# Optimization experiments

Hardware: AMD Instinct MI355X
Metric: run time of the kernel (lower is better)

Reference implementation:

```python
import jax, jax.numpy as jnp
import numpy as np

IN_F, OUT_F, NG = 2048, 8192, 16
EPS = 1e-5

def setup_inputs() -> dict:
    key = jax.random.key(0)
    k = jax.random.split(key, 6)
    x = jax.random.normal(k[0], (4096, IN_F), dtype=jnp.float32)
    W = jax.random.normal(k[1], (OUT_F, IN_F), dtype=jnp.float32) * (1.0 / np.sqrt(IN_F))
    b = jax.random.normal(k[2], (OUT_F,), dtype=jnp.float32) * 0.01
    gn_w = jnp.ones((OUT_F,), dtype=jnp.float32)
    gn_b = jnp.zeros((OUT_F,), dtype=jnp.float32)
    mult_w = jax.random.normal(k[3], (OUT_F,), dtype=jnp.float32)
    return {"x": x, "W": W, "b": b, "gn_w": gn_w, "gn_b": gn_b, "mult_w": mult_w}

def reference(x, W, b, gn_w, gn_b, mult_w):
    B = x.shape[0]
    y = x @ W.T + b  # [B, OUT_F]
    g = y.reshape(B, NG, OUT_F // NG)
    mean = jnp.mean(g, axis=-1, keepdims=True)
    var = jnp.mean(jnp.square(g - mean), axis=-1, keepdims=True)
    n = ((g - mean) * jax.lax.rsqrt(var + EPS)).reshape(B, OUT_F)
    n = n * gn_w + gn_b
    s1 = n * jax.nn.sigmoid(n)
    m = s1 * mult_w
    return m * jax.nn.sigmoid(m)
```

## Files before the change

kernel.cpp:

```cpp
#include <hip/hip_runtime.h>

#define M_DIM 4096
#define N_DIM 8192
#define K_DIM 2048
#define NGRP 16
#define GSZ 512
#define EPSV 1e-5f

#define NX (M_DIM * K_DIM)
#define NW (N_DIM * K_DIM)
#define NY ((size_t)M_DIM * N_DIM)

typedef __attribute__((ext_vector_type(8))) short bf16x8;
typedef __attribute__((ext_vector_type(4))) float f32x4;
typedef __attribute__((ext_vector_type(8))) short shortx8;

__device__ __forceinline__ float b2f(short u) {
    union { unsigned u32; float f; } c;
    c.u32 = ((unsigned)(unsigned short)u) << 16;
    return c.f;
}

__device__ __forceinline__ short f2b(float f) {
    union { float f; unsigned u; } c; c.f = f;
    unsigned r = (c.u + 0x7fffu + ((c.u >> 16) & 1u)) >> 16;
    return (short)r;
}

__global__ __launch_bounds__(256) void convert_kernel(
    const float* __restrict__ x, const float* __restrict__ W,
    short* __restrict__ dst)
{
    const size_t base = ((size_t)blockIdx.x * 256 + threadIdx.x) * 32;
    const float* src = (base < NX) ? (x + base) : (W + (base - NX));
    f32x4 v[8];
#pragma unroll
    for (int c = 0; c < 8; ++c) v[c] = *(const f32x4*)(src + c * 4);
#pragma unroll
    for (int c = 0; c < 4; ++c) {
        shortx8 o;
#pragma unroll
        for (int j = 0; j < 4; ++j) {
            o[j]     = f2b(v[2 * c][j]);
            o[j + 4] = f2b(v[2 * c + 1][j]);
        }
        *(shortx8*)(dst + base + c * 8) = o;
    }
}

#define BKS 32
#define NTILES (K_DIM / BKS)

__global__ __launch_bounds__(512, 2) void gemm256_bf16_kernel(
    const short* __restrict__ A, const short* __restrict__ W, short* __restrict__ C)
{
    __shared__ __align__(16) short lds[4 * 16384];

    const int tid  = threadIdx.x;
    const int lane = tid & 63;
    const int wave = tid >> 6;
    const int wr   = wave >> 2;
    const int wc   = wave & 3;

    const unsigned orig = blockIdx.x;
    const unsigned swz  = (orig & 7) * 64 + (orig >> 3);
    const int blockCol = (swz & 31) * 256;
    const int blockRow = (swz >> 5) * 256;

    const int q0 = tid, q1 = tid + 512;
    const int sr0 = q0 >> 2, sc0 = (q0 & 3) ^ ((q0 >> 3) & 3);
    const int sr1 = q1 >> 2, sc1 = (q1 & 3) ^ ((q1 >> 3) & 3);
    const int offA0 = (blockRow + sr0) * K_DIM + sc0 * 8;
    const int offA1 = (blockRow + sr1) * K_DIM + sc1 * 8;
    const int offB0 = (blockCol + sr0) * K_DIM + sc0 * 8;
    const int offB1 = (blockCol + sr1) * K_DIM + sc1 * 8;

    const int fr    = lane & 15;
    const int pbyte = ((lane >> 4) ^ ((fr >> 1) & 3)) * 16;
    const int aBase = (wr * 128 + fr) * 64 + pbyte;
    const int bBase = (wc * 64  + fr) * 64 + pbyte;

    f32x4 acc[8][4] = {};
    bf16x8 af[8], bf[4];

    auto gll = [&](const short* g, short* l) {
        __builtin_amdgcn_global_load_lds(
            (const __attribute__((address_space(1))) void*)g,
            (__attribute__((address_space(3))) void*)l, 16, 0, 0);
    };
    auto stage1 = [&](int t, int k) {
        short* dA = lds + (t & 3) * 16384;
        short* dB = dA + 8192;
        const int ko = t * BKS;
        if (k == 0)      gll(A + offA0 + ko, dA + q0 * 8);
        else if (k == 1) gll(W + offB0 + ko, dB + q0 * 8);
        else if (k == 2) gll(A + offA1 + ko, dA + q1 * 8);
        else             gll(W + offB1 + ko, dB + q1 * 8);
    };
    auto bar = [&]() {
        __builtin_amdgcn_sched_barrier(0);
        __builtin_amdgcn_s_barrier();
        __builtin_amdgcn_sched_barrier(0);
    };
    auto mf = [&](int ib, int jb) {
        __builtin_amdgcn_s_setprio(1);
#pragma unroll
        for (int i = 0; i < 4; ++i)
#pragma unroll
            for (int j = 0; j < 2; ++j)
                acc[ib + i][jb + j] = __builtin_amdgcn_mfma_f32_16x16x32_bf16(
                    af[ib + i], bf[jb + j], acc[ib + i][jb + j], 0, 0, 0);
        __builtin_amdgcn_s_setprio(0);
    };

    auto subtile = [&](int t, int tstage, bool dostage, int vm) {
        const char* bA = (const char*)lds + (t & 3) * 32768;
        const char* bB = bA + 16384;
        af[0] = *(const bf16x8*)(bA + aBase);
        af[1] = *(const bf16x8*)(bA + aBase + 1024);
        af[2] = *(const bf16x8*)(bA + aBase + 2048);
        af[3] = *(const bf16x8*)(bA + aBase + 3072);
        bf[0] = *(const bf16x8*)(bB + bBase);
        bf[1] = *(const bf16x8*)(bB + bBase + 1024);
        if (dostage) stage1(tstage, 0);
        bar(); mf(0, 0); bar();
        bf[2] = *(const bf16x8*)(bB + bBase + 2048);
        bf[3] = *(const bf16x8*)(bB + bBase + 3072);
        if (dostage) stage1(tstage, 1);
        bar(); mf(0, 2); bar();
        af[4] = *(const bf16x8*)(bA + aBase + 4096);
        af[5] = *(const bf16x8*)(bA + aBase + 5120);
        af[6] = *(const bf16x8*)(bA + aBase + 6144);
        af[7] = *(const bf16x8*)(bA + aBase + 7168);
        if (dostage) stage1(tstage, 2);
        bar(); mf(4, 0); bar();
        if (dostage) stage1(tstage, 3);
        if (vm == 4)      asm volatile("s_waitcnt vmcnt(4)" ::: "memory");
        else if (vm == 0) asm volatile("s_waitcnt vmcnt(0)" ::: "memory");
        bar(); mf(4, 2); bar();
    };

    stage1(0, 0); stage1(0, 1); stage1(0, 2); stage1(0, 3);
    stage1(1, 0); stage1(1, 1); stage1(1, 2); stage1(1, 3);
    asm volatile("s_waitcnt vmcnt(4)" ::: "memory");
    bar();

    for (int i = 0; i < 31; ++i) {
        const int t0 = 2 * i;
        subtile(t0,     t0 + 2, true, 4);
        subtile(t0 + 1, t0 + 3, true, 4);
    }
    subtile(62, 0, false, 0);
    subtile(63, 0, false, -1);

    const int er = (lane >> 4) * 4;
    const int ec = lane & 15;
#pragma unroll
    for (int i = 0; i < 8; ++i) {
        const int rr = blockRow + wr * 128 + i * 16 + er;
#pragma unroll
        for (int j = 0; j < 4; ++j) {
            const int cc = blockCol + wc * 64 + j * 16 + ec;
#pragma unroll
            for (int r = 0; r < 4; ++r)
                C[(size_t)(rr + r) * N_DIM + cc] = f2b(acc[i][j][r]);
        }
    }
}

__global__ __launch_bounds__(256) void gn_silu_bf16_kernel(
    const short* __restrict__ Y,
    const float* __restrict__ bias,
    const float* __restrict__ gnw,
    const float* __restrict__ gnb,
    const float* __restrict__ mw,
    float* __restrict__ out)
{
    const int lane = threadIdx.x & 63;
    const int wave = threadIdx.x >> 6;
    const unsigned gid = blockIdx.x * 4u + wave;
    const unsigned row = gid >> 4;
    const unsigned grp = gid & 15;
    const int col = grp * GSZ + lane * 8;
    const size_t off = (size_t)row * N_DIM + col;

    bf16x8 v = *(const bf16x8*)(Y + off);
    f32x4 b0 = *(const f32x4*)(bias + col);
    f32x4 b1 = *(const f32x4*)(bias + col + 4);

    float y[8];
    float s = 0.f, s2 = 0.f;
#pragma unroll
    for (int j = 0; j < 8; ++j) {
        y[j] = b2f(v[j]) + (j < 4 ? b0[j] : b1[j - 4]);
        s  += y[j];
        s2 += y[j] * y[j];
    }
#pragma unroll
    for (int d = 1; d < 64; d <<= 1) {
        s  += __shfl_xor(s,  d, 64);
        s2 += __shfl_xor(s2, d, 64);
    }
    const float mean = s * (1.0f / GSZ);
    const float var  = s2 * (1.0f / GSZ) - mean * mean;
    const float inv  = rsqrtf(var + EPSV);

    f32x4 w0 = *(const f32x4*)(gnw + col);
    f32x4 w1 = *(const f32x4*)(gnw + col + 4);
    f32x4 g0 = *(const f32x4*)(gnb + col);
    f32x4 g1 = *(const f32x4*)(gnb + col + 4);
    f32x4 m0 = *(const f32x4*)(mw + col);
    f32x4 m1 = *(const f32x4*)(mw + col + 4);

    f32x4 o0, o1;
#pragma unroll
    for (int j = 0; j < 8; ++j) {
        float gwv = j < 4 ? w0[j] : w1[j - 4];
        float gbv = j < 4 ? g0[j] : g1[j - 4];
        float mwv = j < 4 ? m0[j] : m1[j - 4];
        float n  = (y[j] - mean) * inv * gwv + gbv;
        float s1 = n / (1.f + __expf(-n));
        float m  = s1 * mwv;
        float r  = m / (1.f + __expf(-m));
        if (j < 4) o0[j] = r; else o1[j - 4] = r;
    }
    *(f32x4*)(out + off)     = o0;
    *(f32x4*)(out + off + 4) = o1;
}

__global__ __launch_bounds__(256) void gemm_bt_f32_kernel(
    const float* __restrict__ A, const float* __restrict__ W, float* __restrict__ C)
{
    __shared__ __align__(16) short ldsA[128 * 32];
    __shared__ __align__(16) short ldsB[128 * 32];

    const int tid  = threadIdx.x;
    const int lane = tid & 63;
    const int wave = tid >> 6;
    const int blockRow = blockIdx.y * 128;
    const int blockCol = blockIdx.x * 128;
    const int srow = tid >> 1;
    const int scol = (tid & 1) * 16;
    const int wm  = (wave >> 1) * 64;
    const int wn  = (wave & 1) * 64;
    const int fr  = lane & 15;
    const int fko = (lane >> 4) * 8;

    f32x4 acc[4][4] = {};
    const size_t aRowOff = (size_t)(blockRow + srow) * K_DIM;
    const size_t wRowOff = (size_t)(blockCol + srow) * K_DIM;

    for (int k0 = 0; k0 < K_DIM; k0 += 32) {
        f32x4 va0 = *(const f32x4*)(A + aRowOff + k0 + scol);
        f32x4 va1 = *(const f32x4*)(A + aRowOff + k0 + scol + 4);
        f32x4 va2 = *(const f32x4*)(A + aRowOff + k0 + scol + 8);
        f32x4 va3 = *(const f32x4*)(A + aRowOff + k0 + scol + 12);
        f32x4 vb0 = *(const f32x4*)(W + wRowOff + k0 + scol);
        f32x4 vb1 = *(const f32x4*)(W + wRowOff + k0 + scol + 4);
        f32x4 vb2 = *(const f32x4*)(W + wRowOff + k0 + scol + 8);
        f32x4 vb3 = *(const f32x4*)(W + wRowOff + k0 + scol + 12);
        bf16x8 a0, a1, b0, b1;
#pragma unroll
        for (int j = 0; j < 4; ++j) {
            a0[j] = f2b(va0[j]); a0[j + 4] = f2b(va1[j]);
            a1[j] = f2b(va2[j]); a1[j + 4] = f2b(va3[j]);
            b0[j] = f2b(vb0[j]); b0[j + 4] = f2b(vb1[j]);
            b1[j] = f2b(vb2[j]); b1[j + 4] = f2b(vb3[j]);
        }
        *(bf16x8*)(ldsA + srow * 32 + scol)     = a0;
        *(bf16x8*)(ldsA + srow * 32 + scol + 8) = a1;
        *(bf16x8*)(ldsB + srow * 32 + scol)     = b0;
        *(bf16x8*)(ldsB + srow * 32 + scol + 8) = b1;
        __syncthreads();

        bf16x8 af[4], bfv[4];
#pragma unroll
        for (int i = 0; i < 4; ++i) {
            af[i]  = *(const bf16x8*)(ldsA + (wm + i * 16 + fr) * 32 + fko);
            bfv[i] = *(const bf16x8*)(ldsB + (wn + i * 16 + fr) * 32 + fko);
        }
#pragma unroll
        for (int i = 0; i < 4; ++i)
#pragma unroll
            for (int j = 0; j < 4; ++j)
                acc[i][j] = __builtin_amdgcn_mfma_f32_16x16x32_bf16(
                    af[i], bfv[j], acc[i][j], 0, 0, 0);
        __syncthreads();
    }

    const int er = (lane >> 4) * 4;
    const int ec = lane & 15;
#pragma unroll
    for (int i = 0; i < 4; ++i) {
        const int r0 = blockRow + wm + i * 16 + er;
#pragma unroll
        for (int j = 0; j < 4; ++j) {
            const int c0 = blockCol + wn + j * 16 + ec;
#pragma unroll
            for (int r = 0; r < 4; ++r)
                C[(size_t)(r0 + r) * N_DIM + c0] = acc[i][j][r];
        }
    }
}

__global__ __launch_bounds__(256) void gn_silu_f32_kernel(
    float* __restrict__ Y,
    const float* __restrict__ bias,
    const float* __restrict__ gnw,
    const float* __restrict__ gnb,
    const float* __restrict__ mw)
{
    const int lane = threadIdx.x & 63;
    const int wave = threadIdx.x >> 6;
    const unsigned gid = blockIdx.x * 4u + wave;
    const unsigned row = gid >> 4;
    const unsigned grp = gid & 15;
    const int col = grp * GSZ + lane * 8;
    const size_t off = (size_t)row * N_DIM + col;

    f32x4 v0 = *(const f32x4*)(Y + off);
    f32x4 v1 = *(const f32x4*)(Y + off + 4);
    f32x4 b0 = *(const f32x4*)(bias + col);
    f32x4 b1 = *(const f32x4*)(bias + col + 4);

    float y[8];
    float s = 0.f, s2 = 0.f;
#pragma unroll
    for (int j = 0; j < 8; ++j) {
        y[j] = (j < 4 ? v0[j] + b0[j] : v1[j - 4] + b1[j - 4]);
        s += y[j]; s2 += y[j] * y[j];
    }
#pragma unroll
    for (int d = 1; d < 64; d <<= 1) {
        s  += __shfl_xor(s,  d, 64);
        s2 += __shfl_xor(s2, d, 64);
    }
    const float mean = s * (1.0f / GSZ);
    const float var  = s2 * (1.0f / GSZ) - mean * mean;
    const float inv  = rsqrtf(var + EPSV);

    f32x4 w0 = *(const f32x4*)(gnw + col);
    f32x4 w1 = *(const f32x4*)(gnw + col + 4);
    f32x4 g0 = *(const f32x4*)(gnb + col);
    f32x4 g1 = *(const f32x4*)(gnb + col + 4);
    f32x4 m0 = *(const f32x4*)(mw + col);
    f32x4 m1 = *(const f32x4*)(mw + col + 4);

    f32x4 o0, o1;
#pragma unroll
    for (int j = 0; j < 8; ++j) {
        float gwv = j < 4 ? w0[j] : w1[j - 4];
        float gbv = j < 4 ? g0[j] : g1[j - 4];
        float mwv = j < 4 ? m0[j] : m1[j - 4];
        float n  = (y[j] - mean) * inv * gwv + gbv;
        float s1 = n / (1.f + __expf(-n));
        float m  = s1 * mwv;
        float r  = m / (1.f + __expf(-m));
        if (j < 4) o0[j] = r; else o1[j - 4] = r;
    }
    *(f32x4*)(Y + off)     = o0;
    *(f32x4*)(Y + off + 4) = o1;
}

extern "C" void kernel_launch(void* const* d_in, const int* in_sizes, int n_in,
                              void* d_out, int out_size, void* d_ws, size_t ws_size,
                              hipStream_t stream)
{
    const float* x   = (const float*)d_in[0];
    const float* W   = (const float*)d_in[1];
    const float* b   = (const float*)d_in[2];
    const float* gnw = (const float*)d_in[3];
    const float* gnb = (const float*)d_in[4];
    const float* mw  = (const float*)d_in[5];
    float* out = (float*)d_out;

    const size_t need = ((size_t)NX + NW + NY) * sizeof(short);
    const int ngroups = M_DIM * NGRP;

    if (ws_size >= need) {
        short* xb = (short*)d_ws;
        short* Wb = xb + NX;
        short* yb = Wb + NW;

        convert_kernel<<<(NX + NW) / (256 * 32), 256, 0, stream>>>(x, W, xb);
        gemm256_bf16_kernel<<<512, 512, 0, stream>>>(xb, Wb, yb);
        gn_silu_bf16_kernel<<<ngroups / 4, 256, 0, stream>>>(yb, b, gnw, gnb, mw, out);
    } else {
        dim3 ggrid(N_DIM / 128, M_DIM / 128);
        gemm_bt_f32_kernel<<<ggrid, 256, 0, stream>>>(x, W, out);
        gn_silu_f32_kernel<<<ngroups / 4, 256, 0, stream>>>(out, b, gnw, gnb, mw);
    }
}
```

Measured before the change: 370.2 us.

## Coarsen GEMM subtile schedule to two MFMA phases and drop block swizzle

Restructures the inner loop of the bf16 GEMM from four barrier-separated phases of eight MFMAs into two phases of sixteen, loading all B fragments up front and reusing four A fragment registers. It also issues the global-to-LDS stages two at a time and replaces the swizzled 1D block mapping with a plain 2D grid. The aim is fewer barriers and lower register pressure per subtile. The cost is less fine-grained interleaving of loads and compute, and likely worse L2 locality without the block swizzle.

```diff
diff --git a/kernel.cpp b/kernel.cpp
--- a/kernel.cpp
+++ b/kernel.cpp
@@ -61,11 +61,8 @@
     const int wave = tid >> 6;
     const int wr   = wave >> 2;
     const int wc   = wave & 3;
-
-    const unsigned orig = blockIdx.x;
-    const unsigned swz  = (orig & 7) * 64 + (orig >> 3);
-    const int blockCol = (swz & 31) * 256;
-    const int blockRow = (swz >> 5) * 256;
+    const int blockRow = blockIdx.y * 256;
+    const int blockCol = blockIdx.x * 256;
 
     const int q0 = tid, q1 = tid + 512;
     const int sr0 = q0 >> 2, sc0 = (q0 & 3) ^ ((q0 >> 3) & 3);
@@ -81,7 +78,7 @@
     const int bBase = (wc * 64  + fr) * 64 + pbyte;
 
     f32x4 acc[8][4] = {};
-    bf16x8 af[8], bf[4];
+    bf16x8 af[4], bf[4];
 
     auto gll = [&](const short* g, short* l) {
         __builtin_amdgcn_global_load_lds(
@@ -102,16 +99,6 @@
         __builtin_amdgcn_s_barrier();
         __builtin_amdgcn_sched_barrier(0);
     };
-    auto mf = [&](int ib, int jb) {
-        __builtin_amdgcn_s_setprio(1);
-#pragma unroll
-        for (int i = 0; i < 4; ++i)
-#pragma unroll
-            for (int j = 0; j < 2; ++j)
-                acc[ib + i][jb + j] = __builtin_amdgcn_mfma_f32_16x16x32_bf16(
-                    af[ib + i], bf[jb + j], acc[ib + i][jb + j], 0, 0, 0);
-        __builtin_amdgcn_s_setprio(0);
-    };
 
     auto subtile = [&](int t, int tstage, bool dostage, int vm) {
         const char* bA = (const char*)lds + (t & 3) * 32768;
@@ -122,22 +109,36 @@
         af[3] = *(const bf16x8*)(bA + aBase + 3072);
         bf[0] = *(const bf16x8*)(bB + bBase);
         bf[1] = *(const bf16x8*)(bB + bBase + 1024);
-        if (dostage) stage1(tstage, 0);
-        bar(); mf(0, 0); bar();
         bf[2] = *(const bf16x8*)(bB + bBase + 2048);
         bf[3] = *(const bf16x8*)(bB + bBase + 3072);
-        if (dostage) stage1(tstage, 1);
-        bar(); mf(0, 2); bar();
-        af[4] = *(const bf16x8*)(bA + aBase + 4096);
-        af[5] = *(const bf16x8*)(bA + aBase + 5120);
-        af[6] = *(const bf16x8*)(bA + aBase + 6144);
-        af[7] = *(const bf16x8*)(bA + aBase + 7168);
-        if (dostage) stage1(tstage, 2);
-        bar(); mf(4, 0); bar();
-        if (dostage) stage1(tstage, 3);
+        if (dostage) { stage1(tstage, 0); stage1(tstage, 1); }
+        bar();
+        __builtin_amdgcn_s_setprio(1);
+#pragma unroll
+        for (int i = 0; i < 4; ++i)
+#pragma unroll
+            for (int j = 0; j < 4; ++j)
+                acc[i][j] = __builtin_amdgcn_mfma_f32_16x16x32_bf16(
+                    af[i], bf[j], acc[i][j], 0, 0, 0);
+        __builtin_amdgcn_s_setprio(0);
+        bar();
+        af[0] = *(const bf16x8*)(bA + aBase + 4096);
+        af[1] = *(const bf16x8*)(bA + aBase + 5120);
+        af[2] = *(const bf16x8*)(bA + aBase + 6144);
+        af[3] = *(const bf16x8*)(bA + aBase + 7168);
+        if (dostage) { stage1(tstage, 2); stage1(tstage, 3); }
         if (vm == 4)      asm volatile("s_waitcnt vmcnt(4)" ::: "memory");
         else if (vm == 0) asm volatile("s_waitcnt vmcnt(0)" ::: "memory");
-        bar(); mf(4, 2); bar();
+        bar();
+        __builtin_amdgcn_s_setprio(1);
+#pragma unroll
+        for (int i = 0; i < 4; ++i)
+#pragma unroll
+            for (int j = 0; j < 4; ++j)
+                acc[4 + i][j] = __builtin_amdgcn_mfma_f32_16x16x32_bf16(
+                    af[i], bf[j], acc[4 + i][j], 0, 0, 0);
+        __builtin_amdgcn_s_setprio(0);
+        bar();
     };
 
     stage1(0, 0); stage1(0, 1); stage1(0, 2); stage1(0, 3);
@@ -145,11 +146,8 @@
     asm volatile("s_waitcnt vmcnt(4)" ::: "memory");
     bar();
 
-    for (int i = 0; i < 31; ++i) {
-        const int t0 = 2 * i;
-        subtile(t0,     t0 + 2, true, 4);
-        subtile(t0 + 1, t0 + 3, true, 4);
-    }
+    for (int t = 0; t < NTILES - 2; ++t)
+        subtile(t, t + 2, true, 4);
     subtile(62, 0, false, 0);
     subtile(63, 0, false, -1);
 
@@ -383,7 +381,8 @@
         short* yb = Wb + NW;
 
         convert_kernel<<<(NX + NW) / (256 * 32), 256, 0, stream>>>(x, W, xb);
-        gemm256_bf16_kernel<<<512, 512, 0, stream>>>(xb, Wb, yb);
+        dim3 g256(N_DIM / 256, M_DIM / 256);
+        gemm256_bf16_kernel<<<g256, 512, 0, stream>>>(xb, Wb, yb);
         gn_silu_bf16_kernel<<<ngroups / 4, 256, 0, stream>>>(yb, b, gnw, gnb, mw, out);
     } else {
         dim3 ggrid(N_DIM / 128, M_DIM / 128);
```

Measured after the change: 365.1 us. About the same (-1.4%).
